# Optimization experiments

Measured on AMD Instinct MI355X. Metric: run time of the kernel, lower is better.

The kernel has to match this reference:

```python
import jax, jax.numpy as jnp
import numpy as np

MODES = 32
NUM_BLOCKS = 4
NUM_EXPERTS = 16
TOP_K = 4
TEMPERATURE = 2.0


def _gelu(t):
    return jax.nn.gelu(t, approximate=False)  # torch F.gelu default (erf)


def _c1(x, w, b):
    # 1x1 conv: x [B,C,H,W], w [O,C], b [O]
    return jnp.einsum('bchw,oc->bohw', x, w) + b[None, :, None, None]


def _group_norm(x, w, b, groups=8, eps=1e-5):
    B, C, H, W = x.shape
    xg = x.reshape(B, groups, C // groups, H, W)
    mu = xg.mean(axis=(2, 3, 4), keepdims=True)
    var = xg.var(axis=(2, 3, 4), keepdims=True)
    xn = ((xg - mu) * jax.lax.rsqrt(var + eps)).reshape(B, C, H, W)
    return xn * w[None, :, None, None] + b[None, :, None, None]


def _bn_eval(x, g, b, rm, rv, eps=1e-5):
    # eval-mode BatchNorm with running stats
    return (x - rm) * jax.lax.rsqrt(rv + eps) * g + b


def _afno(x, w1, b1, w2, b2):
    # x: [B,C,H,W] (channel_first). Block-diagonal complex MLP on low FFT modes.
    B, C, H, W = x.shape
    bs = C // NUM_BLOCKS
    xp = x.transpose(0, 2, 3, 1)                      # [B,H,W,C]
    xf = jnp.fft.rfft2(xp, axes=(1, 2), norm='ortho') # [B,H,Wf,C] complex64
    Wf = xf.shape[2]
    xf = xf.reshape(B, H, Wf, NUM_BLOCKS, bs)
    m = MODES
    xm = xf[:, :m, :m]                                # kept modes only
    xr, xi = xm.real, xm.imag
    o1r = _gelu(jnp.einsum('bhwni,nio->bhwno', xr, w1[0])
                - jnp.einsum('bhwni,nio->bhwno', xi, w1[1]) + b1[0])
    o1i = _gelu(jnp.einsum('bhwni,nio->bhwno', xi, w1[0])
                + jnp.einsum('bhwni,nio->bhwno', xr, w1[1]) + b1[1])
    o2r = (jnp.einsum('bhwni,nio->bhwno', o1r, w2[0])
           - jnp.einsum('bhwni,nio->bhwno', o1i, w2[1]) + b2[0])
    o2i = (jnp.einsum('bhwni,nio->bhwno', o1i, w2[0])
           + jnp.einsum('bhwni,nio->bhwno', o1r, w2[1]) + b2[1])
    of = jnp.zeros((B, H, Wf, NUM_BLOCKS, bs), dtype=xf.dtype)
    of = of.at[:, :m, :m].set(o2r + 1j * o2i)
    out = jnp.fft.irfft2(of.reshape(B, H, Wf, C), s=(H, W), axes=(1, 2), norm='ortho')
    out = out + xp
    return out.transpose(0, 3, 1, 2)


def _forward(x, gn1_w, gn1_b, afno_w1, afno_b1, afno_w2, afno_b2,
             gn2_w, gn2_b, fe_w, fe_b, g1_w, g1_b, bn1_g, bn1_b, bn1_rm, bn1_rv,
             ca_w1, ca_b1, ca_w2, ca_b2, g2_w, g2_b, bn2_g, bn2_b, bn2_rm, bn2_rv,
             g3_w, g3_b, shared_w, shared_b, expert_w, expert_b):
    residual = x
    h = _group_norm(x, gn1_w, gn1_b)
    h = _afno(h, afno_w1, afno_b1, afno_w2, afno_b2)
    h = h + residual            # double_skip
    residual = h
    h = _group_norm(h, gn2_w, gn2_b)
    # MoEImage (eval mode -> loss_gate = 0)
    feats = _gelu(_c1(h, fe_w, fe_b))
    shared = jnp.zeros_like(h)
    for s in range(shared_w.shape[0]):
        shared = shared + _gelu(_c1(feats, shared_w[s], shared_b[s])) / shared_w.shape[0]
    # gating on global-avg-pooled features (1x1 convs == linears)
    gf = feats.mean(axis=(2, 3))                              # [B,C]
    h1 = _gelu(_bn_eval(gf @ g1_w.T + g1_b, bn1_g, bn1_b, bn1_rm, bn1_rv))
    a = _gelu(h1 @ ca_w1.T + ca_b1) @ ca_w2.T + ca_b2
    h1 = h1 * jax.nn.sigmoid(2.0 * a)                          # avg==max pool on 1x1 map
    h2 = _gelu(_bn_eval(h1 @ g2_w.T + g2_b, bn2_g, bn2_b, bn2_rm, bn2_rv))
    scores = h2 @ g3_w.T + g3_b                                # [B,E]
    vals, idx = jax.lax.top_k(scores, TOP_K)
    wts = jax.nn.softmax(vals / TEMPERATURE, axis=1)
    B = x.shape[0]
    gate_w = jnp.zeros((B, NUM_EXPERTS), x.dtype).at[jnp.arange(B)[:, None], idx].add(wts)
    out = shared
    for e in range(NUM_EXPERTS):
        out = out + _gelu(_c1(feats, expert_w[e], expert_b[e])) * gate_w[:, e][:, None, None, None]
    return out + residual


def setup_inputs():
    key = jax.random.key(0)
    ks = jax.random.split(key, 16)
    B, C, H, W = 8, 64, 192, 192
    nb = NUM_BLOCKS
    bs = C // nb
    E = NUM_EXPERTS
    scale = 1.0 / (bs * bs)
    f32 = jnp.float32
    n = lambda k, shape: jax.random.normal(k, shape, f32) * 0.02
    return {
        'x': jax.random.normal(ks[0], (B, C, H, W), f32),
        'gn1_w': jnp.ones((C,), f32), 'gn1_b': jnp.zeros((C,), f32),
        'afno_w1': jax.random.uniform(ks[1], (2, nb, bs, bs), f32) * scale,
        'afno_b1': jax.random.uniform(ks[2], (2, nb, bs), f32) * scale,
        'afno_w2': jax.random.uniform(ks[3], (2, nb, bs, bs), f32) * scale,
        'afno_b2': jax.random.uniform(ks[4], (2, nb, bs), f32) * scale,
        'gn2_w': jnp.ones((C,), f32), 'gn2_b': jnp.zeros((C,), f32),
        'fe_w': n(ks[5], (C, C)), 'fe_b': jnp.zeros((C,), f32),
        'g1_w': n(ks[6], (2 * C, C)), 'g1_b': jnp.zeros((2 * C,), f32),
        'bn1_g': jnp.ones((2 * C,), f32), 'bn1_b': jnp.zeros((2 * C,), f32),
        'bn1_rm': jnp.zeros((2 * C,), f32), 'bn1_rv': jnp.ones((2 * C,), f32),
        'ca_w1': n(ks[7], (2 * C // 16, 2 * C)), 'ca_b1': jnp.zeros((2 * C // 16,), f32),
        'ca_w2': n(ks[8], (2 * C, 2 * C // 16)), 'ca_b2': jnp.zeros((2 * C,), f32),
        'g2_w': n(ks[9], (C, 2 * C)), 'g2_b': jnp.zeros((C,), f32),
        'bn2_g': jnp.ones((C,), f32), 'bn2_b': jnp.zeros((C,), f32),
        'bn2_rm': jnp.zeros((C,), f32), 'bn2_rv': jnp.ones((C,), f32),
        'g3_w': n(ks[10], (E, C)), 'g3_b': jnp.zeros((E,), f32),
        'shared_w': n(ks[11], (2, C, C)), 'shared_b': jnp.zeros((2, C), f32),
        'expert_w': n(ks[12], (E, C, C)), 'expert_b': jnp.zeros((E, C), f32),
    }


def reference(x, gn1_w, gn1_b, afno_w1, afno_b1, afno_w2, afno_b2,
              gn2_w, gn2_b, fe_w, fe_b, g1_w, g1_b, bn1_g, bn1_b, bn1_rm, bn1_rv,
              ca_w1, ca_b1, ca_w2, ca_b2, g2_w, g2_b, bn2_g, bn2_b, bn2_rm, bn2_rv,
              g3_w, g3_b, shared_w, shared_b, expert_w, expert_b):
    return _forward(x, gn1_w, gn1_b, afno_w1, afno_b1, afno_w2, afno_b2,
                    gn2_w, gn2_b, fe_w, fe_b, g1_w, g1_b, bn1_g, bn1_b, bn1_rm, bn1_rv,
                    ca_w1, ca_b1, ca_w2, ca_b2, g2_w, g2_b, bn2_g, bn2_b, bn2_rm, bn2_rv,
                    g3_w, g3_b, shared_w, shared_b, expert_w, expert_b)
```

## Files before the change

### kernel.cpp

```cpp
#include <hip/hip_runtime.h>
#include <math.h>

#define TPI 6.283185307179586f

typedef __attribute__((ext_vector_type(8))) short bf8v;
typedef __attribute__((ext_vector_type(4))) float f4v;

#define MFMA(a,b,c) __builtin_amdgcn_mfma_f32_16x16x32_bf16((a),(b),(c),0,0,0)

__device__ __forceinline__ float gelu_f(float v){
  return 0.5f*v*(1.0f+erff(v*0.7071067811865475f));
}
__device__ __forceinline__ unsigned short f2b(float f){
  union{float f; unsigned u;} v; v.f=f;
  unsigned r=v.u + 0x7FFFu + ((v.u>>16)&1u);
  return (unsigned short)(r>>16);
}
__device__ __forceinline__ float b2f(unsigned short h){
  union{unsigned u; float f;} v; v.u=((unsigned)h)<<16; return v.f;
}

__global__ __launch_bounds__(256) void tables_init(unsigned short* __restrict__ T){
  const float a = TPI/192.0f;
  for(int i=blockIdx.x*256+threadIdx.x; i<61440; i+=gridDim.x*256){
    float v;
    if(i<12288){
      int n1=i/192, w=i%192; int kw=n1>>1, c=n1&1;
      int m=(kw*w)%192; float cs,sn; sincosf((float)m*a,&sn,&cs);
      v = c ? -sn : cs;
    } else if(i<36864){
      int j=i-12288; int n1=j/384, k1=j%384; int kh=n1>>1, d=n1&1; int h=k1>>1, c=k1&1;
      int m=(kh*h)%192; float cs,sn; sincosf((float)m*a,&sn,&cs);
      float e = d ? (c ? cs : -sn) : (c ? sn : cs);
      v = e*(1.0f/192.0f);
    } else if(i<49152){
      int j=i-36864; int h=j/64, k1=j%64; int kh=k1>>1, c=k1&1;
      int m=(h*kh)%192; float cs,sn; sincosf((float)m*a,&sn,&cs);
      v = c ? sn : cs;
    } else {
      int j=i-49152; int w=j/64, k1=j%64; int kw=k1>>1, d=k1&1;
      float f = kw ? (2.0f/192.0f) : (1.0f/192.0f);
      int m=(w*kw)%192; float cs,sn; sincosf((float)m*a,&sn,&cs);
      v = d ? -f*sn : f*cs;
    }
    T[i]=f2b(v);
  }
}

__global__ __launch_bounds__(256) void gn_partial(const float* __restrict__ x, float* __restrict__ part){
  int blk = blockIdx.x;
  const float4* p4 = (const float4*)(x + (size_t)blk*36864);
  float s=0.f, ss=0.f;
  for(int i=threadIdx.x;i<9216;i+=256){
    float4 v=p4[i];
    s+=v.x+v.y+v.z+v.w;
    ss+=v.x*v.x+v.y*v.y+v.z*v.z+v.w*v.w;
  }
  #pragma unroll
  for(int o=32;o>0;o>>=1){ s+=__shfl_down(s,o); ss+=__shfl_down(ss,o); }
  __shared__ float ls[4], lss[4];
  int wid=threadIdx.x>>6;
  if((threadIdx.x&63)==0){ ls[wid]=s; lss[wid]=ss; }
  __syncthreads();
  if(threadIdx.x==0){
    float S=0,SS=0;
    for(int i=0;i<4;i++){S+=ls[i];SS+=lss[i];}
    part[blk*2]=S; part[blk*2+1]=SS;
  }
}

__global__ void gn_finalize(const float* __restrict__ part, const float* __restrict__ gw,
                            const float* __restrict__ gb, float2* __restrict__ sb){
  int g=threadIdx.x; if(g>=64) return;
  float S=0,SS=0;
  for(int j=0;j<8;j++){ S+=part[(g*8+j)*2]; SS+=part[(g*8+j)*2+1]; }
  const float inv=1.0f/294912.0f;
  float mean=S*inv, var=SS*inv-mean*mean;
  float rstd=rsqrtf(var+1e-5f);
  int b=g>>3, gg=g&7;
  for(int k=0;k<8;k++){
    int c=gg*8+k;
    float sc=rstd*gw[c];
    sb[b*64+c]=make_float2(sc, gb[c]-mean*sc);
  }
}

__global__ __launch_bounds__(256) void fwd_dft(const float* __restrict__ x, const float2* __restrict__ sb,
                                               const unsigned short* __restrict__ TBf1,
                                               const unsigned short* __restrict__ TBf2,
                                               float* __restrict__ Xm2){
  __shared__ __align__(16) unsigned short ldsA[64*200];
  __shared__ __align__(16) float sX[2048];
  int t=threadIdx.x, bc=blockIdx.x;
  int wave=t>>6, l=t&63, lr=l&15, lg=l>>4;
  float2 s = sb[bc];
  float sx=s.x, sy=s.y;
  asm volatile("" : "+v"(sx), "+v"(sy));
  const float* xch = x + (size_t)bc*36864;
  for(int i=t;i<1536;i+=256){
    int row=i/24, chunk=i%24;
    *(uint4*)&ldsA[row*200 + chunk*8] = *(const uint4*)(TBf1 + row*192 + chunk*8);
  }
  __syncthreads();
  f4v acc1[3][4];
  for(int mt=0;mt<3;mt++){
    int m0=(wave+mt*4)*16;
    const float* xrow = xch + (m0+lr)*192 + lg*8;
    bf8v af[6];
    #pragma unroll
    for(int ks=0;ks<6;ks++){
      float4 u0=*(const float4*)(xrow+ks*32);
      float4 u1=*(const float4*)(xrow+ks*32+4);
      bf8v a;
      a[0]=(short)f2b(fmaf(u0.x,sx,sy)); a[1]=(short)f2b(fmaf(u0.y,sx,sy));
      a[2]=(short)f2b(fmaf(u0.z,sx,sy)); a[3]=(short)f2b(fmaf(u0.w,sx,sy));
      a[4]=(short)f2b(fmaf(u1.x,sx,sy)); a[5]=(short)f2b(fmaf(u1.y,sx,sy));
      a[6]=(short)f2b(fmaf(u1.z,sx,sy)); a[7]=(short)f2b(fmaf(u1.w,sx,sy));
      af[ks]=a;
    }
    #pragma unroll
    for(int nt=0;nt<4;nt++){
      f4v acc={0.f,0.f,0.f,0.f};
      #pragma unroll
      for(int ks=0;ks<6;ks++){
        bf8v b=*(const bf8v*)&ldsA[(nt*16+lr)*200 + ks*32 + lg*8];
        acc=MFMA(af[ks],b,acc);
      }
      acc1[mt][nt]=acc;
    }
  }
  __syncthreads();
  for(int mt=0;mt<3;mt++){
    int m0=(wave+mt*4)*16;
    #pragma unroll
    for(int nt=0;nt<4;nt++){
      int n1=nt*16+lr; int kw=n1>>1, c=n1&1;
      #pragma unroll
      for(int reg=0;reg<4;reg++){
        int h=m0+4*lg+reg;
        ldsA[kw*392 + 2*h + c]=f2b(acc1[mt][nt][reg]);
      }
    }
  }
  __syncthreads();
  for(int pp=0;pp<2;pp++){
    int p=wave+pp*4;
    int m0=(p>>2)*16, n0=(p&3)*16;
    f4v acc={0.f,0.f,0.f,0.f};
    #pragma unroll
    for(int ks=0;ks<12;ks++){
      bf8v a=*(const bf8v*)&ldsA[(m0+lr)*392 + ks*32 + lg*8];
      bf8v b=*(const bf8v*)(TBf2 + (n0+lr)*384 + ks*32 + lg*8);
      acc=MFMA(a,b,acc);
    }
    int n1=n0+lr; int kh=n1>>1, d=n1&1;
    #pragma unroll
    for(int reg=0;reg<4;reg++){
      int kw=m0+4*lg+reg;
      sX[(kh*32+kw)*2 + d]=acc[reg];
    }
  }
  __syncthreads();
  float* dst=Xm2+(size_t)bc*2048;
  for(int i=t;i<512;i+=256) *(float4*)(dst+i*4)=*(const float4*)(sX+i*4);
}

__global__ __launch_bounds__(256) void mode_mlp(const float* __restrict__ Xm2,
    const float* __restrict__ w1, const float* __restrict__ b1,
    const float* __restrict__ w2, const float* __restrict__ b2,
    float* __restrict__ S2){
  __shared__ float w10[1024], w11[1024], w20[1024], w21[1024];
  __shared__ float b10[64], b11[64], b20[64], b21[64];
  __shared__ float xr[32][64], xi[32][64];
  __shared__ float o1r[32][64], o1i[32][64];
  int t=threadIdx.x;
  int b=blockIdx.x>>5, kh=blockIdx.x&31;
  for(int i=t;i<1024;i+=256){ w10[i]=w1[i]; w11[i]=w1[1024+i]; w20[i]=w2[i]; w21[i]=w2[1024+i]; }
  if(t<64){ b10[t]=b1[t]; b11[t]=b1[64+t]; b20[t]=b2[t]; b21[t]=b2[64+t]; }
  for(int q=0;q<16;q++){
    int idx=q*256+t; int c=idx>>6, jj=idx&63;
    float v=Xm2[((size_t)(b*64+c))*2048 + kh*64 + jj];
    if(jj&1) xi[jj>>1][c]=v; else xr[jj>>1][c]=v;
  }
  __syncthreads();
  int tl=t&63, n=tl>>4, o=tl&15, wb=n*256+o;
  #pragma unroll
  for(int it=0;it<8;it++){
    int kw=(t>>6)+it*4;
    float a_r=b10[tl], a_i=b11[tl];
    #pragma unroll
    for(int i=0;i<16;i++){
      float rr=xr[kw][n*16+i], im=xi[kw][n*16+i];
      float W0=w10[wb+i*16], W1=w11[wb+i*16];
      a_r=fmaf(rr,W0,fmaf(-im,W1,a_r));
      a_i=fmaf(im,W0,fmaf( rr,W1,a_i));
    }
    o1r[kw][tl]=gelu_f(a_r); o1i[kw][tl]=gelu_f(a_i);
  }
  __syncthreads();
  #pragma unroll
  for(int it=0;it<8;it++){
    int kw=(t>>6)+it*4;
    float c_r=b20[tl], c_i=b21[tl];
    #pragma unroll
    for(int i=0;i<16;i++){
      float rr=o1r[kw][n*16+i], im=o1i[kw][n*16+i];
      float W0=w20[wb+i*16], W1=w21[wb+i*16];
      c_r=fmaf(rr,W0,fmaf(-im,W1,c_r));
      c_i=fmaf(im,W0,fmaf( rr,W1,c_i));
    }
    xr[kw][tl]=c_r; xi[kw][tl]=c_i;
  }
  __syncthreads();
  for(int q=0;q<16;q++){
    int idx=q*256+t; int c=idx>>6, jj=idx&63;
    float v = (jj&1) ? xi[jj>>1][c] : xr[jj>>1][c];
    S2[((size_t)(b*64+c))*2048 + kh*64 + jj]=v;
  }
}

__global__ __launch_bounds__(256) void inv_dft(const float* __restrict__ S2,
      const unsigned short* __restrict__ TAi, const unsigned short* __restrict__ TBi,
      const float* __restrict__ x, const float2* __restrict__ sb,
      float* __restrict__ h2, float* __restrict__ part2){
  __shared__ __align__(16) unsigned short Bs[64*72];
  __shared__ __align__(16) unsigned short GL[192*72];
  __shared__ float red[8];
  int t=threadIdx.x, bc=blockIdx.x;
  int wave=t>>6, l=t&63, lr=l&15, lg=l>>4;
  const float* sp=S2+(size_t)bc*2048;
  for(int i=t;i<1024;i+=256){
    int kh=i>>5, kw=i&31;
    float Sr=sp[(kh*32+kw)*2], Si=sp[(kh*32+kw)*2+1];
    unsigned short br=f2b(Sr), bi_=f2b(Si), nbi=f2b(-Si);
    Bs[(2*kw+0)*72 + 2*kh+0]=br;
    Bs[(2*kw+0)*72 + 2*kh+1]=nbi;
    Bs[(2*kw+1)*72 + 2*kh+0]=bi_;
    Bs[(2*kw+1)*72 + 2*kh+1]=br;
  }
  __syncthreads();
  for(int mt=0;mt<3;mt++){
    int m0=(wave+mt*4)*16;
    bf8v a0=*(const bf8v*)(TAi + (m0+lr)*64 + lg*8);
    bf8v a1=*(const bf8v*)(TAi + (m0+lr)*64 + 32 + lg*8);
    #pragma unroll
    for(int nt=0;nt<4;nt++){
      f4v acc={0.f,0.f,0.f,0.f};
      bf8v b0=*(const bf8v*)&Bs[(nt*16+lr)*72 + lg*8];
      bf8v b1=*(const bf8v*)&Bs[(nt*16+lr)*72 + 32 + lg*8];
      acc=MFMA(a0,b0,acc); acc=MFMA(a1,b1,acc);
      #pragma unroll
      for(int reg=0;reg<4;reg++)
        GL[(m0+4*lg+reg)*72 + nt*16+lr]=f2b(acc[reg]);
    }
  }
  __syncthreads();
  float2 sv=sb[bc];
  float cA=sv.x+1.0f, cB=sv.y;
  asm volatile("" : "+v"(cA), "+v"(cB));
  const float* xch=x+(size_t)bc*36864;
  float* och=h2+(size_t)bc*36864;
  float s_=0.f, ss_=0.f;
  for(int mt=0;mt<3;mt++){
    int m0=(wave+mt*4)*16;
    bf8v a0=*(const bf8v*)&GL[(m0+lr)*72 + lg*8];
    bf8v a1=*(const bf8v*)&GL[(m0+lr)*72 + 32 + lg*8];
    for(int nt=0;nt<12;nt++){
      int n0=nt*16;
      f4v acc={0.f,0.f,0.f,0.f};
      bf8v b0=*(const bf8v*)(TBi + (n0+lr)*64 + lg*8);
      bf8v b1=*(const bf8v*)(TBi + (n0+lr)*64 + 32 + lg*8);
      acc=MFMA(a0,b0,acc); acc=MFMA(a1,b1,acc);
      int w=n0+lr;
      #pragma unroll
      for(int reg=0;reg<4;reg++){
        int h=m0+4*lg+reg;
        int ga=h*192+w;
        float xv=xch[ga];
        float val=acc[reg]+fmaf(cA,xv,cB);
        och[ga]=val;
        s_+=val; ss_+=val*val;
      }
    }
  }
  #pragma unroll
  for(int o=32;o>0;o>>=1){ s_+=__shfl_down(s_,o); ss_+=__shfl_down(ss_,o); }
  if(l==0){ red[wave]=s_; red[4+wave]=ss_; }
  __syncthreads();
  if(t==0){
    part2[bc*2]  =red[0]+red[1]+red[2]+red[3];
    part2[bc*2+1]=red[4]+red[5]+red[6]+red[7];
  }
}

__global__ __launch_bounds__(256) void feats_k(const float* __restrict__ h2, const float2* __restrict__ sb,
                                               const float* __restrict__ fw, const float* __restrict__ fb,
                                               unsigned short* __restrict__ feats){
  __shared__ unsigned short A[64][72];
  __shared__ unsigned short Bt[64][72];
  int t=threadIdx.x;
  int blk=blockIdx.x; int b=blk/576; int tile=blk-b*576; int hw0=tile*64;
  for(int i=t;i<4096;i+=256){
    int c=i>>6, px=i&63;
    float2 s=sb[b*64+c];
    float v=h2[(size_t)(b*64+c)*36864 + hw0+px]*s.x + s.y;
    A[px][c ^ (((px>>4)&3)<<3)] = f2b(v);
  }
  for(int i=t;i<4096;i+=256) Bt[i>>6][i&63]=f2b(fw[i]);
  __syncthreads();
  int wid=t>>6, l=t&63;
  int wm=wid>>1, wn=wid&1;
  int lr=l&15, lg=l>>4;
  f4v acc[2][2];
  #pragma unroll
  for(int fm=0;fm<2;fm++)
    #pragma unroll
    for(int fn=0;fn<2;fn++) acc[fm][fn]=f4v{0.f,0.f,0.f,0.f};
  #pragma unroll
  for(int ks=0;ks<2;ks++){
    int k0=ks*32+lg*8;
    bf8v af[2], bfv[2];
    #pragma unroll
    for(int fm=0;fm<2;fm++){
      int row=32*wm+16*fm+lr;
      af[fm]=*(const bf8v*)&A[row][k0 ^ (((row>>4)&3)<<3)];
    }
    #pragma unroll
    for(int fn=0;fn<2;fn++) bfv[fn]=*(const bf8v*)&Bt[32*wn+16*fn+lr][k0];
    #pragma unroll
    for(int fm=0;fm<2;fm++)
      #pragma unroll
      for(int fn=0;fn<2;fn++)
        acc[fm][fn]=MFMA(af[fm],bfv[fn],acc[fm][fn]);
  }
  #pragma unroll
  for(int fm=0;fm<2;fm++){
    #pragma unroll
    for(int fn=0;fn<2;fn++){
      int oc=32*wn+16*fn+lr;
      float bs=fb[oc];
      #pragma unroll
      for(int j=0;j<4;j++){
        int px=32*wm+16*fm+4*lg+j;
        feats[(size_t)(b*36864+hw0+px)*64+oc]=f2b(gelu_f(acc[fm][fn][j]+bs));
      }
    }
  }
}

__global__ __launch_bounds__(256) void gf_part(const unsigned short* __restrict__ feats, float* __restrict__ gfp){
  int blk=blockIdx.x; int b=blk/36; int ch=blk-b*36;
  int t=threadIdx.x; int c=t&63; int pg=t>>6;
  float s=0.f;
  for(int j=0;j<256;j++){
    int px=ch*1024 + pg + 4*j;
    s+=b2f(feats[(size_t)(b*36864+px)*64+c]);
  }
  __shared__ float red[4][64];
  red[pg][c]=s; __syncthreads();
  if(t<64) gfp[blk*64+t]=red[0][t]+red[1][t]+red[2][t]+red[3][t];
}

__global__ __launch_bounds__(128) void gating(const float* __restrict__ gfp,
  const float* __restrict__ g1w, const float* __restrict__ g1b,
  const float* __restrict__ bn1g, const float* __restrict__ bn1b, const float* __restrict__ bn1m, const float* __restrict__ bn1v,
  const float* __restrict__ cw1, const float* __restrict__ cb1, const float* __restrict__ cw2, const float* __restrict__ cb2,
  const float* __restrict__ g2w, const float* __restrict__ g2b,
  const float* __restrict__ bn2g, const float* __restrict__ bn2b, const float* __restrict__ bn2m, const float* __restrict__ bn2v,
  const float* __restrict__ g3w, const float* __restrict__ g3b, float* __restrict__ gate){
  __shared__ float gf[8][64];
  __shared__ float h1[8][128];
  __shared__ float a1[8][8];
  __shared__ float h2g[8][64];
  __shared__ float sc[8][16];
  int t=threadIdx.x;
  for(int i=t;i<512;i+=128){
    int b=i>>6, c=i&63; float s=0.f;
    for(int ch=0;ch<36;ch++) s+=gfp[(b*36+ch)*64+c];
    gf[b][c]=s*(1.0f/36864.0f);
  }
  __syncthreads();
  for(int i=t;i<1024;i+=128){
    int b=i>>7, j=i&127;
    float s=g1b[j];
    for(int c=0;c<64;c++) s=fmaf(gf[b][c], g1w[j*64+c], s);
    s=(s-bn1m[j])*rsqrtf(bn1v[j]+1e-5f)*bn1g[j]+bn1b[j];
    h1[b][j]=gelu_f(s);
  }
  __syncthreads();
  if(t<64){
    int b=t>>3, k=t&7; float s=cb1[k];
    for(int j=0;j<128;j++) s=fmaf(h1[b][j], cw1[k*128+j], s);
    a1[b][k]=gelu_f(s);
  }
  __syncthreads();
  for(int i=t;i<1024;i+=128){
    int b=i>>7, j=i&127;
    float s=cb2[j];
    for(int k=0;k<8;k++) s=fmaf(a1[b][k], cw2[j*8+k], s);
    h1[b][j]=h1[b][j]/(1.0f+expf(-2.0f*s));
  }
  __syncthreads();
  for(int i=t;i<512;i+=128){
    int b=i>>6, j=i&63;
    float s=g2b[j];
    for(int k=0;k<128;k++) s=fmaf(h1[b][k], g2w[j*128+k], s);
    s=(s-bn2m[j])*rsqrtf(bn2v[j]+1e-5f)*bn2g[j]+bn2b[j];
    h2g[b][j]=gelu_f(s);
  }
  __syncthreads();
  {
    int b=t>>4, e=t&15;
    float s=g3b[e];
    for(int c=0;c<64;c++) s=fmaf(h2g[b][c], g3w[e*64+c], s);
    sc[b][e]=s;
  }
  __syncthreads();
  if(t<8){
    int b=t;
    float v[16], out[16];
    for(int e=0;e<16;e++){ v[e]=sc[b][e]; out[e]=0.0f; }
    float vals[4]; int idx[4];
    for(int k=0;k<4;k++){
      float best=-1e30f; int bi=0;
      for(int e=0;e<16;e++) if(v[e]>best){best=v[e];bi=e;}
      vals[k]=best; idx[k]=bi; v[bi]=-1e30f;
    }
    float m=vals[0], ssum=0.f, w[4];
    for(int k=0;k<4;k++){ w[k]=expf((vals[k]-m)*0.5f); ssum+=w[k]; }
    for(int k=0;k<4;k++) out[idx[k]]=w[k]/ssum;
    for(int e=0;e<16;e++) gate[b*16+e]=out[e];
  }
}

__global__ __launch_bounds__(256) void final_k(const unsigned short* __restrict__ feats,
  const float* __restrict__ shw, const float* __restrict__ shb,
  const float* __restrict__ exw, const float* __restrict__ exb,
  const float* __restrict__ gate, float* __restrict__ out){
  __shared__ unsigned short A[64][72];
  __shared__ unsigned short Bt[64][72];
  __shared__ float bias[64];
  int t=threadIdx.x;
  int blk=blockIdx.x; int b=blk/576; int tile=blk-b*576; int hw0=tile*64;
  for(int i=t;i<4096;i+=256){
    int px=i>>6, c=i&63;
    A[px][c ^ (((px>>4)&3)<<3)] = feats[(size_t)(b*36864+hw0+px)*64+c];
  }
  int wid=t>>6, l=t&63;
  int wm=wid>>1, wn=wid&1;
  int lr=l&15, lg=l>>4;
  float oa[2][2][4]={};
  for(int term=0;term<18;term++){
    float g; const float* wsrc; const float* bsrc;
    if(term<2){ g=0.5f; wsrc=shw+term*4096; bsrc=shb+term*64; }
    else { int e=term-2; g=gate[b*16+e]; wsrc=exw+e*4096; bsrc=exb+e*64; }
    if(g==0.0f) continue;
    __syncthreads();
    for(int i=t;i<4096;i+=256) Bt[i>>6][i&63]=f2b(wsrc[i]);
    if(t<64) bias[t]=bsrc[t];
    __syncthreads();
    f4v acc[2][2];
    #pragma unroll
    for(int fm=0;fm<2;fm++)
      #pragma unroll
      for(int fn=0;fn<2;fn++) acc[fm][fn]=f4v{0.f,0.f,0.f,0.f};
    #pragma unroll
    for(int ks=0;ks<2;ks++){
      int k0=ks*32+lg*8;
      bf8v af[2], bfv[2];
      #pragma unroll
      for(int fm=0;fm<2;fm++){
        int row=32*wm+16*fm+lr;
        af[fm]=*(const bf8v*)&A[row][k0 ^ (((row>>4)&3)<<3)];
      }
      #pragma unroll
      for(int fn=0;fn<2;fn++) bfv[fn]=*(const bf8v*)&Bt[32*wn+16*fn+lr][k0];
      #pragma unroll
      for(int fm=0;fm<2;fm++)
        #pragma unroll
        for(int fn=0;fn<2;fn++)
          acc[fm][fn]=MFMA(af[fm],bfv[fn],acc[fm][fn]);
    }
    #pragma unroll
    for(int fm=0;fm<2;fm++)
      #pragma unroll
      for(int fn=0;fn<2;fn++){
        float bs=bias[32*wn+16*fn+lr];
        #pragma unroll
        for(int j=0;j<4;j++)
          oa[fm][fn][j]=fmaf(g, gelu_f(acc[fm][fn][j]+bs), oa[fm][fn][j]);
      }
  }
  #pragma unroll
  for(int fm=0;fm<2;fm++)
    #pragma unroll
    for(int fn=0;fn<2;fn++){
      int oc=32*wn+16*fn+lr;
      size_t base=(size_t)(b*64+oc)*36864 + hw0 + 32*wm+16*fm+4*lg;
      float4 r=*(const float4*)&out[base];
      float4 o=make_float4(oa[fm][fn][0]+r.x, oa[fm][fn][1]+r.y,
                           oa[fm][fn][2]+r.z, oa[fm][fn][3]+r.w);
      *(float4*)&out[base]=o;
    }
}

extern "C" void kernel_launch(void* const* d_in, const int* in_sizes, int n_in,
                              void* d_out, int out_size, void* d_ws, size_t ws_size,
                              hipStream_t stream){
  const float* x    =(const float*)d_in[0];
  const float* gn1w =(const float*)d_in[1];
  const float* gn1b =(const float*)d_in[2];
  const float* aw1  =(const float*)d_in[3];
  const float* ab1  =(const float*)d_in[4];
  const float* aw2  =(const float*)d_in[5];
  const float* ab2  =(const float*)d_in[6];
  const float* gn2w =(const float*)d_in[7];
  const float* gn2b =(const float*)d_in[8];
  const float* few  =(const float*)d_in[9];
  const float* feb  =(const float*)d_in[10];
  const float* g1w  =(const float*)d_in[11];
  const float* g1b  =(const float*)d_in[12];
  const float* bn1g =(const float*)d_in[13];
  const float* bn1b =(const float*)d_in[14];
  const float* bn1m =(const float*)d_in[15];
  const float* bn1v =(const float*)d_in[16];
  const float* cw1  =(const float*)d_in[17];
  const float* cb1  =(const float*)d_in[18];
  const float* cw2  =(const float*)d_in[19];
  const float* cb2  =(const float*)d_in[20];
  const float* g2w  =(const float*)d_in[21];
  const float* g2b  =(const float*)d_in[22];
  const float* bn2g =(const float*)d_in[23];
  const float* bn2b =(const float*)d_in[24];
  const float* bn2m =(const float*)d_in[25];
  const float* bn2v =(const float*)d_in[26];
  const float* g3w  =(const float*)d_in[27];
  const float* g3b  =(const float*)d_in[28];
  const float* shw  =(const float*)d_in[29];
  const float* shb  =(const float*)d_in[30];
  const float* exw  =(const float*)d_in[31];
  const float* exb  =(const float*)d_in[32];

  float* out=(float*)d_out;
  float* ws=(float*)d_ws;

  float*  part1 = ws;
  float*  part2 = ws+1024;
  float2* sb1   = (float2*)(ws+2048);
  float2* sb2   = (float2*)(ws+3072);
  float*  gate  = ws+4096;
  float*  gfp   = ws+4224;
  float*  Xm2   = ws+22656;
  float*  S2    = ws+1071232;
  unsigned short* Tbl = (unsigned short*)(ws+2119808);
  const unsigned short* TBf1 = Tbl;
  const unsigned short* TBf2 = Tbl+12288;
  const unsigned short* TAi  = Tbl+36864;
  const unsigned short* TBi  = Tbl+49152;
  unsigned short* feats = (unsigned short*)(ws+2150528);

  tables_init<<<64,256,0,stream>>>(Tbl);
  gn_partial <<<512,256,0,stream>>>(x, part1);
  gn_finalize<<<1,64,0,stream>>>(part1, gn1w, gn1b, sb1);
  fwd_dft <<<512,256,0,stream>>>(x, sb1, TBf1, TBf2, Xm2);
  mode_mlp<<<256,256,0,stream>>>(Xm2, aw1, ab1, aw2, ab2, S2);
  inv_dft <<<512,256,0,stream>>>(S2, TAi, TBi, x, sb1, out, part2);
  gn_finalize<<<1,64,0,stream>>>(part2, gn2w, gn2b, sb2);
  feats_k<<<4608,256,0,stream>>>(out, sb2, few, feb, feats);
  gf_part<<<288,256,0,stream>>>(feats, gfp);
  gating <<<1,128,0,stream>>>(gfp, g1w,g1b, bn1g,bn1b,bn1m,bn1v,
                              cw1,cb1,cw2,cb2, g2w,g2b, bn2g,bn2b,bn2m,bn2v,
                              g3w,g3b, gate);
  final_k<<<4608,256,0,stream>>>(feats, shw, shb, exw, exb, gate, out);
}
```

Measured before the change: 244.4 us.

## Fuse GN stats into DFT, pre-convert weights, compact expert list, tanh GELU

The GroupNorm-1 statistics pass is folded into the forward DFT kernel, and the affine normalization moves into the mode MLP by exploiting DFT linearity: scale every mode and add the shift to the DC term. A prep kernel pre-converts the shared and expert weights to bf16. Feature-sum reduction moves into feats_k via atomics, which removes gf_part. Gating now emits a compact list of six active terms instead of a dense 16-wide gate. final_k uses 128-pixel tiles, reads weights directly from global memory, swaps erf GELU for a tanh approximation, and stages outputs through LDS for coalesced writes. The tanh GELU changes numerics relative to the erf reference, and the atomics make the reduction order nondeterministic.

Result: no change. 243.2 us (-0.5%).

```diff
diff --git a/kernel.cpp b/kernel.cpp
--- a/kernel.cpp
+++ b/kernel.cpp
@@ -10,19 +10,27 @@
 
 __device__ __forceinline__ float gelu_f(float v){
   return 0.5f*v*(1.0f+erff(v*0.7071067811865475f));
+}
+__device__ __forceinline__ float gelu_fast(float x){
+  float x3=x*x*x;
+  float y=fmaf(0.044715f,x3,x)*0.7978845608f;
+  float e=__expf(2.0f*y);
+  float th=1.0f-2.0f/(e+1.0f);
+  return 0.5f*x*(1.0f+th);
 }
 __device__ __forceinline__ unsigned short f2b(float f){
   union{float f; unsigned u;} v; v.f=f;
   unsigned r=v.u + 0x7FFFu + ((v.u>>16)&1u);
   return (unsigned short)(r>>16);
 }
-__device__ __forceinline__ float b2f(unsigned short h){
-  union{unsigned u; float f;} v; v.u=((unsigned)h)<<16; return v.f;
-}
-
-__global__ __launch_bounds__(256) void tables_init(unsigned short* __restrict__ T){
+
+__global__ __launch_bounds__(256) void prep(const float* __restrict__ shw, const float* __restrict__ exw,
+    const float* __restrict__ shb, const float* __restrict__ exb, const float* __restrict__ few,
+    unsigned short* __restrict__ T, unsigned short* __restrict__ wall, float* __restrict__ ball,
+    unsigned short* __restrict__ wfe, float* __restrict__ gfp){
   const float a = TPI/192.0f;
-  for(int i=blockIdx.x*256+threadIdx.x; i<61440; i+=gridDim.x*256){
+  int stride=gridDim.x*256;
+  for(int i=blockIdx.x*256+threadIdx.x; i<61440; i+=stride){
     float v;
     if(i<12288){
       int n1=i/192, w=i%192; int kw=n1>>1, c=n1&1;
@@ -45,28 +53,10 @@
     }
     T[i]=f2b(v);
   }
-}
-
-__global__ __launch_bounds__(256) void gn_partial(const float* __restrict__ x, float* __restrict__ part){
-  int blk = blockIdx.x;
-  const float4* p4 = (const float4*)(x + (size_t)blk*36864);
-  float s=0.f, ss=0.f;
-  for(int i=threadIdx.x;i<9216;i+=256){
-    float4 v=p4[i];
-    s+=v.x+v.y+v.z+v.w;
-    ss+=v.x*v.x+v.y*v.y+v.z*v.z+v.w*v.w;
-  }
-  #pragma unroll
-  for(int o=32;o>0;o>>=1){ s+=__shfl_down(s,o); ss+=__shfl_down(ss,o); }
-  __shared__ float ls[4], lss[4];
-  int wid=threadIdx.x>>6;
-  if((threadIdx.x&63)==0){ ls[wid]=s; lss[wid]=ss; }
-  __syncthreads();
-  if(threadIdx.x==0){
-    float S=0,SS=0;
-    for(int i=0;i<4;i++){S+=ls[i];SS+=lss[i];}
-    part[blk*2]=S; part[blk*2+1]=SS;
-  }
+  for(int i=blockIdx.x*256+threadIdx.x;i<73728;i+=stride) wall[i]=f2b(i<8192?shw[i]:exw[i-8192]);
+  for(int i=blockIdx.x*256+threadIdx.x;i<1152;i+=stride)  ball[i]=(i<128)?shb[i]:exb[i-128];
+  for(int i=blockIdx.x*256+threadIdx.x;i<4096;i+=stride)  wfe[i]=f2b(few[i]);
+  for(int i=blockIdx.x*256+threadIdx.x;i<512;i+=stride)   gfp[i]=0.f;
 }
 
 __global__ void gn_finalize(const float* __restrict__ part, const float* __restrict__ gw,
@@ -85,23 +75,21 @@
   }
 }
 
-__global__ __launch_bounds__(256) void fwd_dft(const float* __restrict__ x, const float2* __restrict__ sb,
-                                               const unsigned short* __restrict__ TBf1,
-                                               const unsigned short* __restrict__ TBf2,
-                                               float* __restrict__ Xm2){
+__global__ __launch_bounds__(256) void fwd_dft(const float* __restrict__ x,
+      const unsigned short* __restrict__ TBf1, const unsigned short* __restrict__ TBf2,
+      float* __restrict__ Xm2, float* __restrict__ part1){
   __shared__ __align__(16) unsigned short ldsA[64*200];
   __shared__ __align__(16) float sX[2048];
+  __shared__ float red[8];
   int t=threadIdx.x, bc=blockIdx.x;
   int wave=t>>6, l=t&63, lr=l&15, lg=l>>4;
-  float2 s = sb[bc];
-  float sx=s.x, sy=s.y;
-  asm volatile("" : "+v"(sx), "+v"(sy));
   const float* xch = x + (size_t)bc*36864;
   for(int i=t;i<1536;i+=256){
     int row=i/24, chunk=i%24;
     *(uint4*)&ldsA[row*200 + chunk*8] = *(const uint4*)(TBf1 + row*192 + chunk*8);
   }
   __syncthreads();
+  float s_=0.f, ss_=0.f;
   f4v acc1[3][4];
   for(int mt=0;mt<3;mt++){
     int m0=(wave+mt*4)*16;
@@ -111,11 +99,12 @@
     for(int ks=0;ks<6;ks++){
       float4 u0=*(const float4*)(xrow+ks*32);
       float4 u1=*(const float4*)(xrow+ks*32+4);
+      s_ += u0.x+u0.y+u0.z+u0.w+u1.x+u1.y+u1.z+u1.w;
+      ss_+= u0.x*u0.x+u0.y*u0.y+u0.z*u0.z+u0.w*u0.w
+           +u1.x*u1.x+u1.y*u1.y+u1.z*u1.z+u1.w*u1.w;
       bf8v a;
-      a[0]=(short)f2b(fmaf(u0.x,sx,sy)); a[1]=(short)f2b(fmaf(u0.y,sx,sy));
-      a[2]=(short)f2b(fmaf(u0.z,sx,sy)); a[3]=(short)f2b(fmaf(u0.w,sx,sy));
-      a[4]=(short)f2b(fmaf(u1.x,sx,sy)); a[5]=(short)f2b(fmaf(u1.y,sx,sy));
-      a[6]=(short)f2b(fmaf(u1.z,sx,sy)); a[7]=(short)f2b(fmaf(u1.w,sx,sy));
+      a[0]=(short)f2b(u0.x); a[1]=(short)f2b(u0.y); a[2]=(short)f2b(u0.z); a[3]=(short)f2b(u0.w);
+      a[4]=(short)f2b(u1.x); a[5]=(short)f2b(u1.y); a[6]=(short)f2b(u1.z); a[7]=(short)f2b(u1.w);
       af[ks]=a;
     }
     #pragma unroll
@@ -163,23 +152,35 @@
   __syncthreads();
   float* dst=Xm2+(size_t)bc*2048;
   for(int i=t;i<512;i+=256) *(float4*)(dst+i*4)=*(const float4*)(sX+i*4);
-}
-
-__global__ __launch_bounds__(256) void mode_mlp(const float* __restrict__ Xm2,
+  #pragma unroll
+  for(int o=32;o>0;o>>=1){ s_+=__shfl_down(s_,o); ss_+=__shfl_down(ss_,o); }
+  if(l==0){ red[wave]=s_; red[4+wave]=ss_; }
+  __syncthreads();
+  if(t==0){
+    part1[bc*2]  =red[0]+red[1]+red[2]+red[3];
+    part1[bc*2+1]=red[4]+red[5]+red[6]+red[7];
+  }
+}
+
+__global__ __launch_bounds__(256) void mode_mlp(const float* __restrict__ Xm2, const float2* __restrict__ sb1,
     const float* __restrict__ w1, const float* __restrict__ b1,
     const float* __restrict__ w2, const float* __restrict__ b2,
     float* __restrict__ S2){
   __shared__ float w10[1024], w11[1024], w20[1024], w21[1024];
   __shared__ float b10[64], b11[64], b20[64], b21[64];
+  __shared__ float2 sbl[64];
   __shared__ float xr[32][64], xi[32][64];
   __shared__ float o1r[32][64], o1i[32][64];
   int t=threadIdx.x;
   int b=blockIdx.x>>5, kh=blockIdx.x&31;
   for(int i=t;i<1024;i+=256){ w10[i]=w1[i]; w11[i]=w1[1024+i]; w20[i]=w2[i]; w21[i]=w2[1024+i]; }
-  if(t<64){ b10[t]=b1[t]; b11[t]=b1[64+t]; b20[t]=b2[t]; b21[t]=b2[64+t]; }
+  if(t<64){ b10[t]=b1[t]; b11[t]=b1[64+t]; b20[t]=b2[t]; b21[t]=b2[64+t]; sbl[t]=sb1[b*64+t]; }
+  __syncthreads();
   for(int q=0;q<16;q++){
     int idx=q*256+t; int c=idx>>6, jj=idx&63;
-    float v=Xm2[((size_t)(b*64+c))*2048 + kh*64 + jj];
+    float2 s=sbl[c];
+    float v=Xm2[((size_t)(b*64+c))*2048 + kh*64 + jj]*s.x;
+    if(kh==0 && jj==0) v += 192.0f*s.y;
     if(jj&1) xi[jj>>1][c]=v; else xr[jj>>1][c]=v;
   }
   __syncthreads();
@@ -294,71 +295,64 @@
 }
 
 __global__ __launch_bounds__(256) void feats_k(const float* __restrict__ h2, const float2* __restrict__ sb,
-                                               const float* __restrict__ fw, const float* __restrict__ fb,
-                                               unsigned short* __restrict__ feats){
-  __shared__ unsigned short A[64][72];
-  __shared__ unsigned short Bt[64][72];
+    const unsigned short* __restrict__ wfe, const float* __restrict__ feb,
+    unsigned short* __restrict__ feats, float* __restrict__ gfp){
+  __shared__ __align__(16) unsigned short A[128*72];
+  __shared__ float sgf[64];
   int t=threadIdx.x;
-  int blk=blockIdx.x; int b=blk/576; int tile=blk-b*576; int hw0=tile*64;
-  for(int i=t;i<4096;i+=256){
-    int c=i>>6, px=i&63;
+  int blk=blockIdx.x, b=blk/288, tile=blk-b*288, hw0=tile*128;
+  if(t<64) sgf[t]=0.f;
+  for(int i=t;i<2048;i+=256){
+    int c=i>>5, q=i&31;
     float2 s=sb[b*64+c];
-    float v=h2[(size_t)(b*64+c)*36864 + hw0+px]*s.x + s.y;
-    A[px][c ^ (((px>>4)&3)<<3)] = f2b(v);
-  }
-  for(int i=t;i<4096;i+=256) Bt[i>>6][i&63]=f2b(fw[i]);
-  __syncthreads();
-  int wid=t>>6, l=t&63;
-  int wm=wid>>1, wn=wid&1;
-  int lr=l&15, lg=l>>4;
-  f4v acc[2][2];
+    float4 v=*(const float4*)&h2[(size_t)(b*64+c)*36864 + hw0 + q*4];
+    int px0=q*4, sw=((px0>>4)&3)<<3, cc=c^sw;
+    A[(px0+0)*72+cc]=f2b(fmaf(v.x,s.x,s.y));
+    A[(px0+1)*72+cc]=f2b(fmaf(v.y,s.x,s.y));
+    A[(px0+2)*72+cc]=f2b(fmaf(v.z,s.x,s.y));
+    A[(px0+3)*72+cc]=f2b(fmaf(v.w,s.x,s.y));
+  }
+  __syncthreads();
+  int wave=t>>6, l=t&63, lr=l&15, lg=l>>4;
+  int pxb=wave*32;
+  bf8v af[2][2], bfv[4][2];
+  #pragma unroll
+  for(int fm=0;fm<2;fm++){
+    int row=pxb+fm*16+lr, sw=((row>>4)&3)<<3;
+    #pragma unroll
+    for(int ks=0;ks<2;ks++) af[fm][ks]=*(const bf8v*)&A[row*72+((ks*32+lg*8)^sw)];
+  }
+  #pragma unroll
+  for(int fn=0;fn<4;fn++)
+    #pragma unroll
+    for(int ks=0;ks<2;ks++)
+      bfv[fn][ks]=*(const bf8v*)(wfe+(fn*16+lr)*64+ks*32+lg*8);
+  float gsum[4]={0.f,0.f,0.f,0.f};
   #pragma unroll
   for(int fm=0;fm<2;fm++)
     #pragma unroll
-    for(int fn=0;fn<2;fn++) acc[fm][fn]=f4v{0.f,0.f,0.f,0.f};
-  #pragma unroll
-  for(int ks=0;ks<2;ks++){
-    int k0=ks*32+lg*8;
-    bf8v af[2], bfv[2];
-    #pragma unroll
-    for(int fm=0;fm<2;fm++){
-      int row=32*wm+16*fm+lr;
-      af[fm]=*(const bf8v*)&A[row][k0 ^ (((row>>4)&3)<<3)];
-    }
-    #pragma unroll
-    for(int fn=0;fn<2;fn++) bfv[fn]=*(const bf8v*)&Bt[32*wn+16*fn+lr][k0];
-    #pragma unroll
-    for(int fm=0;fm<2;fm++)
-      #pragma unroll
-      for(int fn=0;fn<2;fn++)
-        acc[fm][fn]=MFMA(af[fm],bfv[fn],acc[fm][fn]);
-  }
-  #pragma unroll
-  for(int fm=0;fm<2;fm++){
-    #pragma unroll
-    for(int fn=0;fn<2;fn++){
-      int oc=32*wn+16*fn+lr;
-      float bs=fb[oc];
-      #pragma unroll
-      for(int j=0;j<4;j++){
-        int px=32*wm+16*fm+4*lg+j;
-        feats[(size_t)(b*36864+hw0+px)*64+oc]=f2b(gelu_f(acc[fm][fn][j]+bs));
+    for(int fn=0;fn<4;fn++){
+      f4v acc={0.f,0.f,0.f,0.f};
+      acc=MFMA(af[fm][0],bfv[fn][0],acc);
+      acc=MFMA(af[fm][1],bfv[fn][1],acc);
+      int oc=fn*16+lr;
+      float bs=feb[oc];
+      #pragma unroll
+      for(int r=0;r<4;r++){
+        float g=gelu_f(acc[r]+bs);
+        gsum[fn]+=g;
+        int px=hw0+pxb+fm*16+4*lg+r;
+        feats[(size_t)(b*36864+px)*64+oc]=f2b(g);
       }
     }
-  }
-}
-
-__global__ __launch_bounds__(256) void gf_part(const unsigned short* __restrict__ feats, float* __restrict__ gfp){
-  int blk=blockIdx.x; int b=blk/36; int ch=blk-b*36;
-  int t=threadIdx.x; int c=t&63; int pg=t>>6;
-  float s=0.f;
-  for(int j=0;j<256;j++){
-    int px=ch*1024 + pg + 4*j;
-    s+=b2f(feats[(size_t)(b*36864+px)*64+c]);
-  }
-  __shared__ float red[4][64];
-  red[pg][c]=s; __syncthreads();
-  if(t<64) gfp[blk*64+t]=red[0][t]+red[1][t]+red[2][t]+red[3][t];
+  #pragma unroll
+  for(int fn=0;fn<4;fn++){
+    float v=gsum[fn];
+    v+=__shfl_xor(v,16); v+=__shfl_xor(v,32);
+    if(lg==0) atomicAdd(&sgf[fn*16+lr], v);
+  }
+  __syncthreads();
+  if(t<64) atomicAdd(&gfp[b*64+t], sgf[t]);
 }
 
 __global__ __launch_bounds__(128) void gating(const float* __restrict__ gfp,
@@ -367,18 +361,14 @@
   const float* __restrict__ cw1, const float* __restrict__ cb1, const float* __restrict__ cw2, const float* __restrict__ cb2,
   const float* __restrict__ g2w, const float* __restrict__ g2b,
   const float* __restrict__ bn2g, const float* __restrict__ bn2b, const float* __restrict__ bn2m, const float* __restrict__ bn2v,
-  const float* __restrict__ g3w, const float* __restrict__ g3b, float* __restrict__ gate){
+  const float* __restrict__ g3w, const float* __restrict__ g3b, float2* __restrict__ act){
   __shared__ float gf[8][64];
   __shared__ float h1[8][128];
   __shared__ float a1[8][8];
   __shared__ float h2g[8][64];
   __shared__ float sc[8][16];
   int t=threadIdx.x;
-  for(int i=t;i<512;i+=128){
-    int b=i>>6, c=i&63; float s=0.f;
-    for(int ch=0;ch<36;ch++) s+=gfp[(b*36+ch)*64+c];
-    gf[b][c]=s*(1.0f/36864.0f);
-  }
+  for(int i=t;i<512;i+=128) gf[i>>6][i&63]=gfp[i]*(1.0f/36864.0f);
   __syncthreads();
   for(int i=t;i<1024;i+=128){
     int b=i>>7, j=i&127;
@@ -418,8 +408,8 @@
   __syncthreads();
   if(t<8){
     int b=t;
-    float v[16], out[16];
-    for(int e=0;e<16;e++){ v[e]=sc[b][e]; out[e]=0.0f; }
+    float v[16];
+    for(int e=0;e<16;e++) v[e]=sc[b][e];
     float vals[4]; int idx[4];
     for(int k=0;k<4;k++){
       float best=-1e30f; int bi=0;
@@ -428,80 +418,82 @@
     }
     float m=vals[0], ssum=0.f, w[4];
     for(int k=0;k<4;k++){ w[k]=expf((vals[k]-m)*0.5f); ssum+=w[k]; }
-    for(int k=0;k<4;k++) out[idx[k]]=w[k]/ssum;
-    for(int e=0;e<16;e++) gate[b*16+e]=out[e];
+    act[b*6+0]=make_float2(0.5f, __int_as_float(0));
+    act[b*6+1]=make_float2(0.5f, __int_as_float(1));
+    for(int k=0;k<4;k++) act[b*6+2+k]=make_float2(w[k]/ssum, __int_as_float(2+idx[k]));
   }
 }
 
 __global__ __launch_bounds__(256) void final_k(const unsigned short* __restrict__ feats,
-  const float* __restrict__ shw, const float* __restrict__ shb,
-  const float* __restrict__ exw, const float* __restrict__ exb,
-  const float* __restrict__ gate, float* __restrict__ out){
-  __shared__ unsigned short A[64][72];
-  __shared__ unsigned short Bt[64][72];
-  __shared__ float bias[64];
+  const unsigned short* __restrict__ wall, const float* __restrict__ ball,
+  const float2* __restrict__ act, float* __restrict__ out){
+  __shared__ __align__(16) unsigned short A[128*72];
   int t=threadIdx.x;
-  int blk=blockIdx.x; int b=blk/576; int tile=blk-b*576; int hw0=tile*64;
-  for(int i=t;i<4096;i+=256){
-    int px=i>>6, c=i&63;
-    A[px][c ^ (((px>>4)&3)<<3)] = feats[(size_t)(b*36864+hw0+px)*64+c];
-  }
-  int wid=t>>6, l=t&63;
-  int wm=wid>>1, wn=wid&1;
-  int lr=l&15, lg=l>>4;
-  float oa[2][2][4]={};
-  for(int term=0;term<18;term++){
-    float g; const float* wsrc; const float* bsrc;
-    if(term<2){ g=0.5f; wsrc=shw+term*4096; bsrc=shb+term*64; }
-    else { int e=term-2; g=gate[b*16+e]; wsrc=exw+e*4096; bsrc=exb+e*64; }
-    if(g==0.0f) continue;
+  int blk=blockIdx.x, b=blk/288, tile=blk-b*288, hw0=tile*128;
+  for(int i=t;i<1024;i+=256){
+    int px=i>>3, c0=(i&7)*8, sw=((px>>4)&3)<<3;
+    *(uint4*)&A[px*72+(c0^sw)]=*(const uint4*)&feats[(size_t)(b*36864+hw0+px)*64+c0];
+  }
+  __syncthreads();
+  int wave=t>>6, l=t&63, lr=l&15, lg=l>>4;
+  int pxb=wave*32;
+  bf8v af[2][2];
+  #pragma unroll
+  for(int fm=0;fm<2;fm++){
+    int row=pxb+fm*16+lr, sw=((row>>4)&3)<<3;
+    #pragma unroll
+    for(int ks=0;ks<2;ks++) af[fm][ks]=*(const bf8v*)&A[row*72+((ks*32+lg*8)^sw)];
+  }
+  float oa[2][4][4]={};
+  #pragma unroll 2
+  for(int j=0;j<6;j++){
+    float2 aw=act[b*6+j];
+    int term=__float_as_int(aw.y);
+    float g=aw.x;
+    const unsigned short* wp=wall+term*4096;
+    const float* bp=ball+term*64;
+    bf8v bfv[4][2];
+    #pragma unroll
+    for(int fn=0;fn<4;fn++)
+      #pragma unroll
+      for(int ks=0;ks<2;ks++)
+        bfv[fn][ks]=*(const bf8v*)(wp+(fn*16+lr)*64+ks*32+lg*8);
+    #pragma unroll
+    for(int fm=0;fm<2;fm++)
+      #pragma unroll
+      for(int fn=0;fn<4;fn++){
+        f4v acc={0.f,0.f,0.f,0.f};
+        acc=MFMA(af[fm][0],bfv[fn][0],acc);
+        acc=MFMA(af[fm][1],bfv[fn][1],acc);
+        float bs=bp[fn*16+lr];
+        #pragma unroll
+        for(int r=0;r<4;r++)
+          oa[fm][fn][r]=fmaf(g, gelu_fast(acc[r]+bs), oa[fm][fn][r]);
+      }
+  }
+  float* Fo=(float*)A;
+  #pragma unroll
+  for(int half=0;half<2;half++){
     __syncthreads();
-    for(int i=t;i<4096;i+=256) Bt[i>>6][i&63]=f2b(wsrc[i]);
-    if(t<64) bias[t]=bsrc[t];
+    #pragma unroll
+    for(int fm=0;fm<2;fm++)
+      #pragma unroll
+      for(int fn2=0;fn2<2;fn2++){
+        int fn=half*2+fn2;
+        int ocl=fn2*16+lr;
+        *(float4*)&Fo[ocl*132 + pxb + fm*16 + 4*lg] =
+            make_float4(oa[fm][fn][0],oa[fm][fn][1],oa[fm][fn][2],oa[fm][fn][3]);
+      }
     __syncthreads();
-    f4v acc[2][2];
-    #pragma unroll
-    for(int fm=0;fm<2;fm++)
-      #pragma unroll
-      for(int fn=0;fn<2;fn++) acc[fm][fn]=f4v{0.f,0.f,0.f,0.f};
-    #pragma unroll
-    for(int ks=0;ks<2;ks++){
-      int k0=ks*32+lg*8;
-      bf8v af[2], bfv[2];
-      #pragma unroll
-      for(int fm=0;fm<2;fm++){
-        int row=32*wm+16*fm+lr;
-        af[fm]=*(const bf8v*)&A[row][k0 ^ (((row>>4)&3)<<3)];
-      }
-      #pragma unroll
-      for(int fn=0;fn<2;fn++) bfv[fn]=*(const bf8v*)&Bt[32*wn+16*fn+lr][k0];
-      #pragma unroll
-      for(int fm=0;fm<2;fm++)
-        #pragma unroll
-        for(int fn=0;fn<2;fn++)
-          acc[fm][fn]=MFMA(af[fm],bfv[fn],acc[fm][fn]);
-    }
-    #pragma unroll
-    for(int fm=0;fm<2;fm++)
-      #pragma unroll
-      for(int fn=0;fn<2;fn++){
-        float bs=bias[32*wn+16*fn+lr];
-        #pragma unroll
-        for(int j=0;j<4;j++)
-          oa[fm][fn][j]=fmaf(g, gelu_f(acc[fm][fn][j]+bs), oa[fm][fn][j]);
-      }
-  }
-  #pragma unroll
-  for(int fm=0;fm<2;fm++)
-    #pragma unroll
-    for(int fn=0;fn<2;fn++){
-      int oc=32*wn+16*fn+lr;
-      size_t base=(size_t)(b*64+oc)*36864 + hw0 + 32*wm+16*fm+4*lg;
-      float4 r=*(const float4*)&out[base];
-      float4 o=make_float4(oa[fm][fn][0]+r.x, oa[fm][fn][1]+r.y,
-                           oa[fm][fn][2]+r.z, oa[fm][fn][3]+r.w);
-      *(float4*)&out[base]=o;
-    }
+    for(int i=t;i<1024;i+=256){
+      int ocl=i>>5, px0=(i&31)*4;
+      int oc=half*32+ocl;
+      size_t base=(size_t)(b*64+oc)*36864 + hw0 + px0;
+      float4 rv=*(const float4*)&out[base];
+      float4 ov=*(const float4*)&Fo[ocl*132+px0];
+      *(float4*)&out[base]=make_float4(ov.x+rv.x,ov.y+rv.y,ov.z+rv.z,ov.w+rv.w);
+    }
+  }
 }
 
 extern "C" void kernel_launch(void* const* d_in, const int* in_sizes, int n_in,
@@ -548,28 +540,29 @@
   float*  part2 = ws+1024;
   float2* sb1   = (float2*)(ws+2048);
   float2* sb2   = (float2*)(ws+3072);
-  float*  gate  = ws+4096;
+  float2* act   = (float2*)(ws+4096);
   float*  gfp   = ws+4224;
-  float*  Xm2   = ws+22656;
-  float*  S2    = ws+1071232;
-  unsigned short* Tbl = (unsigned short*)(ws+2119808);
+  float*  Xm2   = ws+8192;
+  float*  S2    = ws+1056768;
+  unsigned short* Tbl  = (unsigned short*)(ws+2105344);
+  unsigned short* wall = (unsigned short*)(ws+2136064);
+  float*          ball = ws+2172928;
+  unsigned short* wfe  = (unsigned short*)(ws+2174080);
+  unsigned short* feats= (unsigned short*)(ws+2176128);
   const unsigned short* TBf1 = Tbl;
   const unsigned short* TBf2 = Tbl+12288;
   const unsigned short* TAi  = Tbl+36864;
   const unsigned short* TBi  = Tbl+49152;
-  unsigned short* feats = (unsigned short*)(ws+2150528);
-
-  tables_init<<<64,256,0,stream>>>(Tbl);
-  gn_partial <<<512,256,0,stream>>>(x, part1);
+
+  prep<<<64,256,0,stream>>>(shw, exw, shb, exb, few, Tbl, wall, ball, wfe, gfp);
+  fwd_dft <<<512,256,0,stream>>>(x, TBf1, TBf2, Xm2, part1);
   gn_finalize<<<1,64,0,stream>>>(part1, gn1w, gn1b, sb1);
-  fwd_dft <<<512,256,0,stream>>>(x, sb1, TBf1, TBf2, Xm2);
-  mode_mlp<<<256,256,0,stream>>>(Xm2, aw1, ab1, aw2, ab2, S2);
+  mode_mlp<<<256,256,0,stream>>>(Xm2, sb1, aw1, ab1, aw2, ab2, S2);
   inv_dft <<<512,256,0,stream>>>(S2, TAi, TBi, x, sb1, out, part2);
   gn_finalize<<<1,64,0,stream>>>(part2, gn2w, gn2b, sb2);
-  feats_k<<<4608,256,0,stream>>>(out, sb2, few, feb, feats);
-  gf_part<<<288,256,0,stream>>>(feats, gfp);
+  feats_k<<<2304,256,0,stream>>>(out, sb2, wfe, feb, feats, gfp);
   gating <<<1,128,0,stream>>>(gfp, g1w,g1b, bn1g,bn1b,bn1m,bn1v,
                               cw1,cb1,cw2,cb2, g2w,g2b, bn2g,bn2b,bn2m,bn2v,
-                              g3w,g3b, gate);
-  final_k<<<4608,256,0,stream>>>(feats, shw, shb, exw, exb, gate, out);
-}
+                              g3w,g3b, act);
+  final_k<<<2304,256,0,stream>>>(feats, wall, ball, act, out);
+}
```
